# Optimization experiments

Hardware: AMD Instinct MI355X
Metric: run time of the kernel (lower is better)

The kernel has to match this reference:

```python
import jax, jax.numpy as jnp
import numpy as np

DIM = 1024
NHEAD = 16
HEAD_DIM = DIM // NHEAD


def setup_inputs() -> dict:
    key = jax.random.key(0)
    k_x, k_wqkv, k_bqkv, k_wp, k_bp = jax.random.split(key, 5)
    scale = 1.0 / np.sqrt(DIM)
    return {
        "x": jax.random.normal(k_x, (4, 2048, DIM), dtype=jnp.float32),
        "w_qkv": jax.random.uniform(k_wqkv, (DIM, 3 * DIM), minval=-scale, maxval=scale, dtype=jnp.float32),
        "b_qkv": jax.random.uniform(k_bqkv, (3 * DIM,), minval=-scale, maxval=scale, dtype=jnp.float32),
        "w_proj": jax.random.uniform(k_wp, (DIM, DIM), minval=-scale, maxval=scale, dtype=jnp.float32),
        "b_proj": jax.random.uniform(k_bp, (DIM,), minval=-scale, maxval=scale, dtype=jnp.float32),
    }


def reference(x, w_qkv, b_qkv, w_proj, b_proj):
    B, N, D = x.shape
    # qkv projection: [B,N,3D] -> [3,B,H,N,hd]
    qkv = x @ w_qkv + b_qkv
    qkv = qkv.reshape(B, N, 3, NHEAD, HEAD_DIM).transpose(2, 0, 3, 1, 4)
    q, k, v = qkv[0], qkv[1], qkv[2]
    # naive full attention: scores [B,H,N,N]
    attn = jnp.einsum("bhqd,bhkd->bhqk", q, k) / jnp.sqrt(jnp.float32(HEAD_DIM))
    attn = jax.nn.softmax(attn, axis=-1)
    out = jnp.einsum("bhqk,bhkd->bhqd", attn, v)  # [B,H,N,hd]
    out = out.transpose(0, 2, 1, 3).reshape(B, N, D)
    return out @ w_proj + b_proj
```

## Files before the change

kernel.cpp:

```cpp
#include <hip/hip_runtime.h>
#include <math.h>

#define DIM     1024
#define NHEAD   16
#define HD      64
#define BATCH   4
#define SEQ     2048
#define MTOT    (BATCH * SEQ)
#define QKV_N   (3 * DIM)

typedef __attribute__((ext_vector_type(8))) short bf16x8;
typedef __attribute__((ext_vector_type(4))) float f32x4;
typedef unsigned int u32;
typedef unsigned short u16;

__device__ __forceinline__ u16 f2bf(float f) {
    u32 u = __float_as_uint(f);
    return (u16)((u + 0x7fffu + ((u >> 16) & 1u)) >> 16);
}

__device__ __forceinline__ float exp2_fast(float x) {
    float r; asm("v_exp_f32 %0, %1" : "=v"(r) : "v"(x)); return r;
}

__device__ __forceinline__ u32 cvtpk_bf16(float lo, float hi) {
    u32 r; asm("v_cvt_pk_bf16_f32 %0, %1, %2" : "=v"(r) : "v"(lo), "v"(hi));
    return r;
}

__device__ __forceinline__ void gload_lds16(const u16* g, u16* l) {
    __builtin_amdgcn_global_load_lds((const __attribute__((address_space(1))) u32*)g,
                                     (__attribute__((address_space(3))) u32*)l, 16, 0, 0);
}

__global__ __launch_bounds__(256) void cast_x(const float* __restrict__ in,
                                              u16* __restrict__ out) {
    const int i = (blockIdx.x * 256 + threadIdx.x) * 4;
    const float4 v = *(const float4*)&in[i];
    ushort4 o;
    o.x = f2bf(v.x); o.y = f2bf(v.y); o.z = f2bf(v.z); o.w = f2bf(v.w);
    *(ushort4*)&out[i] = o;
}

__global__ __launch_bounds__(256) void cast_transpose(const float* __restrict__ W,
                                                      u16* __restrict__ Wt,
                                                      int K, int N) {
    __shared__ float Ls[64][65];
    const int k0 = blockIdx.x * 64, n0 = blockIdx.y * 64;
    const int t = threadIdx.x;
    const int r = t >> 4, c4 = (t & 15) << 2;
    #pragma unroll
    for (int i = 0; i < 4; ++i) {
        const float4 v = *(const float4*)&W[(size_t)(k0 + r + i * 16) * N + n0 + c4];
        Ls[r + i * 16][c4 + 0] = v.x; Ls[r + i * 16][c4 + 1] = v.y;
        Ls[r + i * 16][c4 + 2] = v.z; Ls[r + i * 16][c4 + 3] = v.w;
    }
    __syncthreads();
    #pragma unroll
    for (int i = 0; i < 4; ++i) {
        const int nr = r + i * 16;
        ushort4 o;
        o.x = f2bf(Ls[c4 + 0][nr]); o.y = f2bf(Ls[c4 + 1][nr]);
        o.z = f2bf(Ls[c4 + 2][nr]); o.w = f2bf(Ls[c4 + 3][nr]);
        *(ushort4*)&Wt[(size_t)(n0 + nr) * K + k0 + c4] = o;
    }
}

#define GEMM_STAGE(buf, kof, Aptr, Bptr)                                       \
    _Pragma("unroll") for (int i = 0; i < 2; ++i) {                            \
        const int row = w * 32 + i * 16 + (lane >> 2);                         \
        const int slot = (lane & 3) ^ ((row >> 1) & 3);                        \
        gload_lds16(&Aptr[(size_t)(m0 + row) * DIM + (kof) + slot * 8],        \
                    &As[buf][(w * 32 + i * 16) * 32]);                         \
        gload_lds16(&Bptr[(size_t)(n0 + row) * DIM + (kof) + slot * 8],        \
                    &Bs[buf][(w * 32 + i * 16) * 32]);                         \
    }

#define GEMM_MAINLOOP(Aptr, Bptr)                                              \
    __shared__ __align__(16) u16 As[2][128 * 32];                              \
    __shared__ __align__(16) u16 Bs[2][128 * 32];                              \
    const int t = threadIdx.x;                                                 \
    const int lane = t & 63, w = t >> 6;                                       \
    const int n0 = blockIdx.x * 128;                                           \
    const int m0 = blockIdx.y * 128;                                           \
    const int wm = (w & 1) * 64, wn = (w >> 1) * 64;                           \
    const int g = lane >> 4, li = lane & 15;                                   \
    f32x4 acc[4][4];                                                           \
    _Pragma("unroll") for (int mt = 0; mt < 4; ++mt)                           \
        _Pragma("unroll") for (int nt = 0; nt < 4; ++nt)                       \
            acc[mt][nt] = (f32x4){0.f, 0.f, 0.f, 0.f};                         \
    GEMM_STAGE(0, 0, Aptr, Bptr)                                               \
    __syncthreads();                                                           \
    int cur = 0;                                                               \
    for (int k0 = 0; k0 < DIM; k0 += 32) {                                     \
        if (k0 + 32 < DIM) { GEMM_STAGE(cur ^ 1, k0 + 32, Aptr, Bptr) }        \
        bf16x8 a[4], b[4];                                                     \
        _Pragma("unroll") for (int mt = 0; mt < 4; ++mt) {                     \
            const int row = wm + mt * 16 + li;                                 \
            const int slot = g ^ ((row >> 1) & 3);                             \
            a[mt] = *(const bf16x8*)&As[cur][row * 32 + slot * 8];             \
        }                                                                      \
        _Pragma("unroll") for (int nt = 0; nt < 4; ++nt) {                     \
            const int row = wn + nt * 16 + li;                                 \
            const int slot = g ^ ((row >> 1) & 3);                             \
            b[nt] = *(const bf16x8*)&Bs[cur][row * 32 + slot * 8];             \
        }                                                                      \
        _Pragma("unroll") for (int mt = 0; mt < 4; ++mt)                       \
            _Pragma("unroll") for (int nt = 0; nt < 4; ++nt)                   \
                acc[mt][nt] = __builtin_amdgcn_mfma_f32_16x16x32_bf16(         \
                    a[mt], b[nt], acc[mt][nt], 0, 0, 0);                       \
        __syncthreads();                                                       \
        cur ^= 1;                                                              \
    }

#define QSCALE 0.18033688011112042f
__global__ __launch_bounds__(256) void gemm_qkv(
    const u16* __restrict__ A, const u16* __restrict__ Bt,
    const float* __restrict__ bias,
    u16* __restrict__ qo, u16* __restrict__ ko, u16* __restrict__ vo)
{
    GEMM_MAINLOOP(A, Bt)
    #pragma unroll
    for (int nt = 0; nt < 4; ++nt) {
        const int n = n0 + wn + nt * 16 + li;
        const int which = n >> 10;
        const int head  = (n >> 6) & 15;
        const int hd    = n & 63;
        u16* dst = (which == 0) ? qo : (which == 1) ? ko : vo;
        const float scale = (which == 0) ? QSCALE : 1.0f;
        const float bv = bias[n];
        #pragma unroll
        for (int mt = 0; mt < 4; ++mt) {
            #pragma unroll
            for (int r = 0; r < 4; ++r) {
                const int m = m0 + wm + mt * 16 + g * 4 + r;
                const int bb = m >> 11, tok = m & 2047;
                dst[((size_t)(bb * NHEAD + head) * SEQ + tok) * HD + hd] =
                    f2bf((acc[mt][nt][r] + bv) * scale);
            }
        }
    }
}

__global__ __launch_bounds__(256) void gemm_proj(
    const u16* __restrict__ A, const u16* __restrict__ Bt,
    const float* __restrict__ bias, float* __restrict__ out)
{
    GEMM_MAINLOOP(A, Bt)
    #pragma unroll
    for (int nt = 0; nt < 4; ++nt) {
        const int n = n0 + wn + nt * 16 + li;
        const float bv = bias[n];
        #pragma unroll
        for (int mt = 0; mt < 4; ++mt) {
            #pragma unroll
            for (int r = 0; r < 4; ++r) {
                const int m = m0 + wm + mt * 16 + g * 4 + r;
                out[(size_t)m * DIM + n] = acc[mt][nt][r] + bv;
            }
        }
    }
}

#define LSTR 72
#define NKT  (SEQ / 64)
__global__ __launch_bounds__(256) void attn_mfma(
    const u16* __restrict__ q, const u16* __restrict__ k,
    const u16* __restrict__ v, u16* __restrict__ ao)
{
    __shared__ __align__(16) u16 Ks[64 * LSTR];
    __shared__ __align__(16) u16 Vt[64 * LSTR];
    __shared__ __align__(16) u16 Ps[4 * 32 * LSTR];

    const int t = threadIdx.x;
    const int lane = t & 63, w = t >> 6;
    const int g = lane >> 4, li = lane & 15;
    const int q0 = blockIdx.x * 128;
    const int bh = blockIdx.y;
    const size_t base = (size_t)bh * SEQ * HD;

    bf16x8 qf[2][2];
    #pragma unroll
    for (int h = 0; h < 2; ++h) {
        const size_t qrow = base + (size_t)(q0 + w * 32 + h * 16 + li) * HD;
        qf[h][0] = *(const bf16x8*)&q[qrow + g * 8];
        qf[h][1] = *(const bf16x8*)&q[qrow + 32 + g * 8];
    }

    float lsum[2] = {0.f, 0.f};
    f32x4 oacc[2][4];
    #pragma unroll
    for (int h = 0; h < 2; ++h)
        #pragma unroll
        for (int nt = 0; nt < 4; ++nt) oacc[h][nt] = (f32x4){0.f, 0.f, 0.f, 0.f};

    u16* Pw = &Ps[w * 32 * LSTR];

    const int kk = t >> 2,        kh  = (t & 3) << 4;
    const int vkey = (t & 31) << 1, vh0 = (t >> 5) << 3;

    bf16x8 rk0, rk1, rv0, rv1;
    {
        const size_t kb = base;
        rk0 = *(const bf16x8*)&k[kb + (size_t)kk * HD + kh];
        rk1 = *(const bf16x8*)&k[kb + (size_t)kk * HD + kh + 8];
        rv0 = *(const bf16x8*)&v[kb + (size_t)vkey * HD + vh0];
        rv1 = *(const bf16x8*)&v[kb + (size_t)(vkey + 1) * HD + vh0];
    }

    for (int kt = 0; kt < NKT; ++kt) {
        *(bf16x8*)&Ks[kk * LSTR + kh]     = rk0;
        *(bf16x8*)&Ks[kk * LSTR + kh + 8] = rk1;
        #pragma unroll
        for (int i = 0; i < 8; ++i) {
            const u32 pk = (u32)(u16)rv0[i] | ((u32)(u16)rv1[i] << 16);
            *(u32*)&Vt[(vh0 + i) * LSTR + vkey] = pk;
        }
        __syncthreads();

        if (kt + 1 < NKT) {
            const size_t kb = base + (size_t)(kt + 1) * 64 * HD;
            rk0 = *(const bf16x8*)&k[kb + (size_t)kk * HD + kh];
            rk1 = *(const bf16x8*)&k[kb + (size_t)kk * HD + kh + 8];
            rv0 = *(const bf16x8*)&v[kb + (size_t)vkey * HD + vh0];
            rv1 = *(const bf16x8*)&v[kb + (size_t)(vkey + 1) * HD + vh0];
        }

        f32x4 s[2][4];
        __builtin_amdgcn_s_setprio(1);
        #pragma unroll
        for (int nt = 0; nt < 4; ++nt) {
            const bf16x8 kf0 = *(const bf16x8*)&Ks[(nt * 16 + li) * LSTR + g * 8];
            const bf16x8 kf1 = *(const bf16x8*)&Ks[(nt * 16 + li) * LSTR + 32 + g * 8];
            #pragma unroll
            for (int h = 0; h < 2; ++h) {
                f32x4 c = (f32x4){0.f, 0.f, 0.f, 0.f};
                c = __builtin_amdgcn_mfma_f32_16x16x32_bf16(kf0, qf[h][0], c, 0, 0, 0);
                c = __builtin_amdgcn_mfma_f32_16x16x32_bf16(kf1, qf[h][1], c, 0, 0, 0);
                s[h][nt] = c;
            }
        }
        __builtin_amdgcn_s_setprio(0);

        #pragma unroll
        for (int h = 0; h < 2; ++h) {
            float rs = 0.f;
            #pragma unroll
            for (int nt = 0; nt < 4; ++nt)
                #pragma unroll
                for (int r = 0; r < 4; ++r) {
                    const float p = exp2_fast(s[h][nt][r]);
                    s[h][nt][r] = p;
                    rs += p;
                }
            lsum[h] += rs;
            #pragma unroll
            for (int nt = 0; nt < 4; ++nt) {
                uint2 w2;
                w2.x = cvtpk_bf16(s[h][nt][0], s[h][nt][1]);
                w2.y = cvtpk_bf16(s[h][nt][2], s[h][nt][3]);
                *(uint2*)&Pw[(h * 16 + li) * LSTR + nt * 16 + (g << 2)] = w2;
            }
        }

        asm volatile("s_waitcnt lgkmcnt(0)" ::: "memory");
        __builtin_amdgcn_sched_barrier(0);

        __builtin_amdgcn_s_setprio(1);
        #pragma unroll
        for (int ks = 0; ks < 2; ++ks) {
            bf16x8 vb[4];
            #pragma unroll
            for (int nt = 0; nt < 4; ++nt)
                vb[nt] = *(const bf16x8*)&Vt[(nt * 16 + li) * LSTR + ks * 32 + g * 8];
            #pragma unroll
            for (int h = 0; h < 2; ++h) {
                const bf16x8 pa = *(const bf16x8*)&Pw[(h * 16 + li) * LSTR + ks * 32 + g * 8];
                #pragma unroll
                for (int nt = 0; nt < 4; ++nt)
                    oacc[h][nt] = __builtin_amdgcn_mfma_f32_16x16x32_bf16(
                        pa, vb[nt], oacc[h][nt], 0, 0, 0);
            }
        }
        __builtin_amdgcn_s_setprio(0);
        __syncthreads();
    }

    const int bb = bh >> 4, hd = bh & 15;
    #pragma unroll
    for (int h = 0; h < 2; ++h) {
        float lf = lsum[h];
        lf += __shfl_xor(lf, 16);
        lf += __shfl_xor(lf, 32);
        #pragma unroll
        for (int r = 0; r < 4; ++r) {
            const float lr = __shfl(lf, (lane & 48) + (g << 2) + r);
            const float inv = 1.0f / lr;
            const int tok = q0 + w * 32 + h * 16 + (g << 2) + r;
            #pragma unroll
            for (int nt = 0; nt < 4; ++nt)
                ao[((size_t)(bb * SEQ + tok)) * DIM + hd * HD + nt * 16 + li] =
                    f2bf(oacc[h][nt][r] * inv);
        }
    }
}

extern "C" void kernel_launch(void* const* d_in, const int* in_sizes, int n_in,
                              void* d_out, int out_size, void* d_ws, size_t ws_size,
                              hipStream_t stream)
{
    const float* x      = (const float*)d_in[0];
    const float* w_qkv  = (const float*)d_in[1];
    const float* b_qkv  = (const float*)d_in[2];
    const float* w_proj = (const float*)d_in[3];
    const float* b_proj = (const float*)d_in[4];
    float* out = (float*)d_out;

    u16* xb  = (u16*)d_ws;
    u16* wqt = xb  + (size_t)MTOT * DIM;
    u16* wpt = wqt + (size_t)QKV_N * DIM;
    u16* qb  = wpt + (size_t)DIM * DIM;
    u16* kb  = qb  + (size_t)MTOT * DIM;
    u16* vb  = kb  + (size_t)MTOT * DIM;
    u16* aob = vb  + (size_t)MTOT * DIM;

    cast_x<<<(MTOT * DIM) / 1024, 256, 0, stream>>>(x, xb);
    cast_transpose<<<dim3(DIM / 64, QKV_N / 64), 256, 0, stream>>>(w_qkv, wqt, DIM, QKV_N);
    cast_transpose<<<dim3(DIM / 64, DIM / 64), 256, 0, stream>>>(w_proj, wpt, DIM, DIM);

    gemm_qkv<<<dim3(QKV_N / 128, MTOT / 128), 256, 0, stream>>>(xb, wqt, b_qkv, qb, kb, vb);
    attn_mfma<<<dim3(SEQ / 128, BATCH * NHEAD), 256, 0, stream>>>(qb, kb, vb, aob);
    gemm_proj<<<dim3(DIM / 128, MTOT / 128), 256, 0, stream>>>(aob, wpt, b_proj, out);
}
```

Measured before the change: 217.3 us.

## Keep P in registers via permuted K rows and double-buffer K/V tiles

Loads K rows in a permuted order so the S accumulator layout lines up directly with the B-operand fragment layout of the PV MFMA. The P tile stays in registers and is no longer round-tripped through LDS. K/V tiles are double-buffered in shared memory, so one barrier per iteration covers both the writes for the next tile and the reads of the current one. The output is now written as packed 32-bit stores. This trades more LDS for K/V for removing the P store/load traffic and a sync, and it drops the setprio hints.

```diff
diff --git a/kernel.cpp b/kernel.cpp
--- a/kernel.cpp
+++ b/kernel.cpp
@@ -168,9 +168,8 @@
     const u16* __restrict__ q, const u16* __restrict__ k,
     const u16* __restrict__ v, u16* __restrict__ ao)
 {
-    __shared__ __align__(16) u16 Ks[64 * LSTR];
-    __shared__ __align__(16) u16 Vt[64 * LSTR];
-    __shared__ __align__(16) u16 Ps[4 * 32 * LSTR];
+    __shared__ __align__(16) u16 Ks[2][64 * LSTR];
+    __shared__ __align__(16) u16 Vt[2][64 * LSTR];
 
     const int t = threadIdx.x;
     const int lane = t & 63, w = t >> 6;
@@ -194,44 +193,46 @@
         #pragma unroll
         for (int nt = 0; nt < 4; ++nt) oacc[h][nt] = (f32x4){0.f, 0.f, 0.f, 0.f};
 
-    u16* Pw = &Ps[w * 32 * LSTR];
-
-    const int kk = t >> 2,        kh  = (t & 3) << 4;
+    const int kk = t >> 2, kh = (t & 3) << 4;
+    const int kperm = (kk & 32) | (((kk >> 2) & 3) << 3)
+                    | (((kk >> 4) & 1) << 2) | (kk & 3);
     const int vkey = (t & 31) << 1, vh0 = (t >> 5) << 3;
 
     bf16x8 rk0, rk1, rv0, rv1;
+    rk0 = *(const bf16x8*)&k[base + (size_t)kperm * HD + kh];
+    rk1 = *(const bf16x8*)&k[base + (size_t)kperm * HD + kh + 8];
+    rv0 = *(const bf16x8*)&v[base + (size_t)vkey * HD + vh0];
+    rv1 = *(const bf16x8*)&v[base + (size_t)(vkey + 1) * HD + vh0];
     {
-        const size_t kb = base;
-        rk0 = *(const bf16x8*)&k[kb + (size_t)kk * HD + kh];
-        rk1 = *(const bf16x8*)&k[kb + (size_t)kk * HD + kh + 8];
-        rv0 = *(const bf16x8*)&v[kb + (size_t)vkey * HD + vh0];
-        rv1 = *(const bf16x8*)&v[kb + (size_t)(vkey + 1) * HD + vh0];
-    }
-
-    for (int kt = 0; kt < NKT; ++kt) {
-        *(bf16x8*)&Ks[kk * LSTR + kh]     = rk0;
-        *(bf16x8*)&Ks[kk * LSTR + kh + 8] = rk1;
+        u16* Kn = Ks[0]; u16* Vn = Vt[0];
+        *(bf16x8*)&Kn[kk * LSTR + kh]     = rk0;
+        *(bf16x8*)&Kn[kk * LSTR + kh + 8] = rk1;
         #pragma unroll
         for (int i = 0; i < 8; ++i) {
             const u32 pk = (u32)(u16)rv0[i] | ((u32)(u16)rv1[i] << 16);
-            *(u32*)&Vt[(vh0 + i) * LSTR + vkey] = pk;
-        }
-        __syncthreads();
-
-        if (kt + 1 < NKT) {
+            *(u32*)&Vn[(vh0 + i) * LSTR + vkey] = pk;
+        }
+    }
+    __syncthreads();
+
+    int cur = 0;
+    for (int kt = 0; kt < NKT; ++kt) {
+        const bool more = (kt + 1 < NKT);
+        if (more) {
             const size_t kb = base + (size_t)(kt + 1) * 64 * HD;
-            rk0 = *(const bf16x8*)&k[kb + (size_t)kk * HD + kh];
-            rk1 = *(const bf16x8*)&k[kb + (size_t)kk * HD + kh + 8];
+            rk0 = *(const bf16x8*)&k[kb + (size_t)kperm * HD + kh];
+            rk1 = *(const bf16x8*)&k[kb + (size_t)kperm * HD + kh + 8];
             rv0 = *(const bf16x8*)&v[kb + (size_t)vkey * HD + vh0];
             rv1 = *(const bf16x8*)&v[kb + (size_t)(vkey + 1) * HD + vh0];
         }
+        const u16* Kc = Ks[cur];
+        const u16* Vc = Vt[cur];
 
         f32x4 s[2][4];
-        __builtin_amdgcn_s_setprio(1);
         #pragma unroll
         for (int nt = 0; nt < 4; ++nt) {
-            const bf16x8 kf0 = *(const bf16x8*)&Ks[(nt * 16 + li) * LSTR + g * 8];
-            const bf16x8 kf1 = *(const bf16x8*)&Ks[(nt * 16 + li) * LSTR + 32 + g * 8];
+            const bf16x8 kf0 = *(const bf16x8*)&Kc[(nt * 16 + li) * LSTR + g * 8];
+            const bf16x8 kf1 = *(const bf16x8*)&Kc[(nt * 16 + li) * LSTR + 32 + g * 8];
             #pragma unroll
             for (int h = 0; h < 2; ++h) {
                 f32x4 c = (f32x4){0.f, 0.f, 0.f, 0.f};
@@ -240,8 +241,8 @@
                 s[h][nt] = c;
             }
         }
-        __builtin_amdgcn_s_setprio(0);
-
+
+        bf16x8 pb[2][2];
         #pragma unroll
         for (int h = 0; h < 2; ++h) {
             float rs = 0.f;
@@ -255,52 +256,57 @@
                 }
             lsum[h] += rs;
             #pragma unroll
+            for (int ks = 0; ks < 2; ++ks) {
+                union { u32 u[4]; bf16x8 v8; } uu;
+                uu.u[0] = cvtpk_bf16(s[h][2 * ks][0],     s[h][2 * ks][1]);
+                uu.u[1] = cvtpk_bf16(s[h][2 * ks][2],     s[h][2 * ks][3]);
+                uu.u[2] = cvtpk_bf16(s[h][2 * ks + 1][0], s[h][2 * ks + 1][1]);
+                uu.u[3] = cvtpk_bf16(s[h][2 * ks + 1][2], s[h][2 * ks + 1][3]);
+                pb[h][ks] = uu.v8;
+            }
+        }
+
+        #pragma unroll
+        for (int ks = 0; ks < 2; ++ks) {
+            #pragma unroll
             for (int nt = 0; nt < 4; ++nt) {
-                uint2 w2;
-                w2.x = cvtpk_bf16(s[h][nt][0], s[h][nt][1]);
-                w2.y = cvtpk_bf16(s[h][nt][2], s[h][nt][3]);
-                *(uint2*)&Pw[(h * 16 + li) * LSTR + nt * 16 + (g << 2)] = w2;
-            }
-        }
-
-        asm volatile("s_waitcnt lgkmcnt(0)" ::: "memory");
-        __builtin_amdgcn_sched_barrier(0);
-
-        __builtin_amdgcn_s_setprio(1);
-        #pragma unroll
-        for (int ks = 0; ks < 2; ++ks) {
-            bf16x8 vb[4];
-            #pragma unroll
-            for (int nt = 0; nt < 4; ++nt)
-                vb[nt] = *(const bf16x8*)&Vt[(nt * 16 + li) * LSTR + ks * 32 + g * 8];
-            #pragma unroll
-            for (int h = 0; h < 2; ++h) {
-                const bf16x8 pa = *(const bf16x8*)&Pw[(h * 16 + li) * LSTR + ks * 32 + g * 8];
+                const bf16x8 vb = *(const bf16x8*)&Vc[(nt * 16 + li) * LSTR + ks * 32 + g * 8];
                 #pragma unroll
-                for (int nt = 0; nt < 4; ++nt)
+                for (int h = 0; h < 2; ++h)
                     oacc[h][nt] = __builtin_amdgcn_mfma_f32_16x16x32_bf16(
-                        pa, vb[nt], oacc[h][nt], 0, 0, 0);
-            }
-        }
-        __builtin_amdgcn_s_setprio(0);
+                        vb, pb[h][ks], oacc[h][nt], 0, 0, 0);
+            }
+        }
+
+        if (more) {
+            u16* Kn = Ks[cur ^ 1]; u16* Vn = Vt[cur ^ 1];
+            *(bf16x8*)&Kn[kk * LSTR + kh]     = rk0;
+            *(bf16x8*)&Kn[kk * LSTR + kh + 8] = rk1;
+            #pragma unroll
+            for (int i = 0; i < 8; ++i) {
+                const u32 pk = (u32)(u16)rv0[i] | ((u32)(u16)rv1[i] << 16);
+                *(u32*)&Vn[(vh0 + i) * LSTR + vkey] = pk;
+            }
+        }
         __syncthreads();
-    }
-
-    const int bb = bh >> 4, hd = bh & 15;
+        cur ^= 1;
+    }
+
+    const int bb = bh >> 4, hh = bh & 15;
     #pragma unroll
     for (int h = 0; h < 2; ++h) {
         float lf = lsum[h];
         lf += __shfl_xor(lf, 16);
         lf += __shfl_xor(lf, 32);
-        #pragma unroll
-        for (int r = 0; r < 4; ++r) {
-            const float lr = __shfl(lf, (lane & 48) + (g << 2) + r);
-            const float inv = 1.0f / lr;
-            const int tok = q0 + w * 32 + h * 16 + (g << 2) + r;
-            #pragma unroll
-            for (int nt = 0; nt < 4; ++nt)
-                ao[((size_t)(bb * SEQ + tok)) * DIM + hd * HD + nt * 16 + li] =
-                    f2bf(oacc[h][nt][r] * inv);
+        const float inv = 1.0f / lf;
+        const int tok = q0 + w * 32 + h * 16 + li;
+        u16* dst = &ao[(size_t)(bb * SEQ + tok) * DIM + hh * HD];
+        #pragma unroll
+        for (int nt = 0; nt < 4; ++nt) {
+            const u32 p0 = cvtpk_bf16(oacc[h][nt][0] * inv, oacc[h][nt][1] * inv);
+            const u32 p1 = cvtpk_bf16(oacc[h][nt][2] * inv, oacc[h][nt][3] * inv);
+            *(u32*)&dst[nt * 16 + g * 4]     = p0;
+            *(u32*)&dst[nt * 16 + g * 4 + 2] = p1;
         }
     }
 }
```

Result: faster. 205.9 us (-5.2%).
